# Performance work log

Hardware: AMD Instinct MI355X
Metric: run time of the kernel (lower is better)

The kernel has to match this reference:

```python
import jax, jax.numpy as jnp
import numpy as np

VOCAB = 100000
SHORTLIST = 10000  # cutoffs = [10000, 20000, 40000, 80000], n_clusters = 4
B, T, D = 1024, 128, 1024


def setup_inputs() -> dict:
    key = jax.random.key(0)
    ks = jax.random.split(key, 12)
    s = 0.02  # realistic init scale for weights
    inp = {
        "features": jax.random.normal(ks[0], (B, D), jnp.float32),
        "head_weight": jax.random.normal(ks[1], (SHORTLIST + 4, D), jnp.float32) * s,
        "proj0": jax.random.normal(ks[2], (512, D), jnp.float32) * s,
        "out0": jax.random.normal(ks[3], (10000, 512), jnp.float32) * s,
        "proj1": jax.random.normal(ks[4], (256, D), jnp.float32) * s,
        "out1": jax.random.normal(ks[5], (20000, 256), jnp.float32) * s,
        "proj2": jax.random.normal(ks[6], (128, D), jnp.float32) * s,
        "out2": jax.random.normal(ks[7], (40000, 128), jnp.float32) * s,
        "proj3": jax.random.normal(ks[8], (64, D), jnp.float32) * s,
        "out3": jax.random.normal(ks[9], (20000, 64), jnp.float32) * s,
        "discard_probs": jax.random.uniform(ks[10], (VOCAB,), jnp.float32),
        "targets": jax.random.randint(ks[11], (B, T), 0, VOCAB, jnp.int64),
        "target_mask": jnp.ones((B, T), jnp.bool_),
    }
    return inp


def _adaptive_log_prob(x, head_weight, projs, outs):
    # head: shortlist logits + one logit per tail cluster
    head_lp = jax.nn.log_softmax(x @ head_weight.T, axis=-1)  # [B, SHORTLIST+4]
    parts = [head_lp[:, :SHORTLIST]]
    for i, (pw, ow) in enumerate(zip(projs, outs)):
        cluster_logits = (x @ pw.T) @ ow.T  # [B, osz]
        parts.append(jax.nn.log_softmax(cluster_logits, axis=-1)
                     + head_lp[:, SHORTLIST + i:SHORTLIST + i + 1])
    return jnp.concatenate(parts, axis=-1)  # [B, VOCAB]


def reference(features, head_weight, proj0, out0, proj1, out1, proj2, out2,
              proj3, out3, discard_probs, targets, target_mask):
    # dropout is identity in eval/reference mode
    logprob = _adaptive_log_prob(features, head_weight,
                                 (proj0, proj1, proj2, proj3),
                                 (out0, out1, out2, out3))
    lp_t = jnp.take_along_axis(logprob, targets, axis=1)        # [B, T]
    w = (1.0 - discard_probs[targets]) * target_mask.astype(lp_t.dtype)
    per_sample = jnp.sum(-lp_t * w, axis=1) / jnp.sum(w, axis=1)  # [B]
    return jnp.sum(per_sample) / (targets.shape[0] + 1e-5)
```

## Files before the change

kernel.cpp:

```cpp
#include <hip/hip_runtime.h>
#include <cstdint>


typedef unsigned short u16;
typedef __attribute__((ext_vector_type(4))) float f32x4;
typedef __attribute__((ext_vector_type(8))) __bf16 bf16x8;
typedef __attribute__((ext_vector_type(4))) unsigned int u32x4;

__device__ __forceinline__ u16 f2bf(float f){
  unsigned u = __float_as_uint(f);
  u += 0x7FFFu + ((u >> 16) & 1u);
  return (u16)(u >> 16);
}

__device__ __forceinline__ float wave_sum(float v){
  #pragma unroll
  for (int d = 1; d < 64; d <<= 1) v += __shfl_xor(v, d, 64);
  return v;
}

__device__ __forceinline__ float wave_dot_l(const u16* a_lds, const u16* b, int len, int lane){
  float s = 0.f;
  for (int k = lane*8; k < len; k += 512){
    u32x4 va = *(const u32x4*)(a_lds + k);
    u32x4 vb = *(const u32x4*)(b + k);
    #pragma unroll
    for (int i = 0; i < 4; i++){
      unsigned ua = va[i], ub = vb[i];
      s = fmaf(__uint_as_float(ua << 16),        __uint_as_float(ub << 16),        s);
      s = fmaf(__uint_as_float(ua & 0xFFFF0000u), __uint_as_float(ub & 0xFFFF0000u), s);
    }
  }
  return wave_sum(s);
}

__device__ __forceinline__ void gload_lds16(const void* g, void* l){
  __builtin_amdgcn_global_load_lds(
      (const __attribute__((address_space(1))) unsigned int*)g,
      (__attribute__((address_space(3))) unsigned int*)l, 16, 0, 0);
}

struct CvtSeg { const float* src; u16* dst; unsigned start; };
struct CvtTab { CvtSeg s[10]; unsigned total; };

__global__ __launch_bounds__(256) void cvt_bf16(CvtTab t){
  unsigned stride = gridDim.x * blockDim.x;
  for (unsigned c = blockIdx.x*blockDim.x + threadIdx.x; c < t.total; c += stride){
    int si = 0;
    #pragma unroll
    for (int i = 1; i < 10; i++) if (c >= t.s[i].start) si = i;
    unsigned lo = c - t.s[si].start;
    const float4* sp = (const float4*)t.s[si].src + (size_t)lo*2;
    float4 f0 = sp[0], f1 = sp[1];
    uint4 d;
    d.x = (unsigned)f2bf(f0.x) | ((unsigned)f2bf(f0.y) << 16);
    d.y = (unsigned)f2bf(f0.z) | ((unsigned)f2bf(f0.w) << 16);
    d.z = (unsigned)f2bf(f1.x) | ((unsigned)f2bf(f1.y) << 16);
    d.w = (unsigned)f2bf(f1.z) | ((unsigned)f2bf(f1.w) << 16);
    ((uint4*)t.s[si].dst)[lo] = d;
  }
}

struct GSeg { const u16* A; const u16* B; float* part; u16* C; float* gates;
              int lda, N, K, ntiles, tileStart, ldc; };
struct GTab { GSeg seg[5]; int nseg; int swz; };

__global__ __launch_bounds__(256, 4) void gemm_all(GTab tab){
  __shared__ __attribute__((aligned(16))) u16 ldsA[128*64];
  __shared__ __attribute__((aligned(16))) u16 ldsB[128*64];
  __shared__ float msLds[128][2];

  int bx = blockIdx.x, by = blockIdx.y;
  if (tab.swz){
    int flat = by * 8 + bx;
    int xcd = flat & 7, j = flat >> 3;
    by = (j >> 3) * 8 + xcd;
    bx = j & 7;
    int nby = (int)gridDim.y;
    if (by >= nby){ by = nby - 1; bx = xcd; }
  }

  int s = 0;
  #pragma unroll
  for (int i = 1; i < 5; i++)
    if (i < tab.nseg && by >= tab.seg[i].tileStart) s = i;
  const u16* Ab = tab.seg[s].A;
  const u16* Bb = tab.seg[s].B;
  float* part   = tab.seg[s].part;
  u16* Cc       = tab.seg[s].C;
  float* gatesp = tab.seg[s].gates;
  int lda = tab.seg[s].lda, N = tab.seg[s].N, K = tab.seg[s].K;
  int ntiles = tab.seg[s].ntiles, ldc = tab.seg[s].ldc;
  int tileN = by - tab.seg[s].tileStart;
  int n0 = tileN * 128;
  int row0 = bx * 128;

  int tid = threadIdx.x;
  int wid = tid >> 6, lane = tid & 63;
  int wr = wid >> 1, wc = wid & 1;
  int qr = lane >> 4, ln = lane & 15;

  const char* baseA = (const char*)(Ab + (size_t)row0*lda);
  const char* baseB = (const char*)Bb;
  unsigned offA[4], offB[4];
  #pragma unroll
  for (int t = 0; t < 4; t++){
    int c = t*256 + tid, row = c >> 3, jj = (c & 7) ^ (row & 7);
    offA[t] = (unsigned)(row*lda + jj*8) * 2u;
    int nr = n0 + row; if (nr >= N) nr = N - 1;
    offB[t] = (unsigned)(nr*K + jj*8) * 2u;
  }
  unsigned ldsWave = (unsigned)(wid << 6) * 16u;

  f32x4 acc[4][4];
  const f32x4 zero = {0.f, 0.f, 0.f, 0.f};
  #pragma unroll
  for (int i = 0; i < 4; i++)
    #pragma unroll
    for (int j = 0; j < 4; j++) acc[i][j] = zero;

  int nkt = K >> 6;
  for (int kt = 0; kt < nkt; kt++){
    __syncthreads();
    unsigned kb = (unsigned)kt * 128u;
    #pragma unroll
    for (int t = 0; t < 4; t++){
      gload_lds16(baseA + offA[t] + kb, (char*)ldsA + (unsigned)t*4096u + ldsWave);
      gload_lds16(baseB + offB[t] + kb, (char*)ldsB + (unsigned)t*4096u + ldsWave);
    }
    __syncthreads();
    #pragma unroll
    for (int ks = 0; ks < 2; ks++){
      bf16x8 av[4], bv[4];
      #pragma unroll
      for (int mt = 0; mt < 4; mt++){
        int rl = wr*64 + mt*16 + ln;
        int ch = rl*8 + ((ks*4 + qr) ^ (rl & 7));
        av[mt] = *(const bf16x8*)((const char*)ldsA + ch*16);
      }
      #pragma unroll
      for (int nt = 0; nt < 4; nt++){
        int rl = wc*64 + nt*16 + ln;
        int ch = rl*8 + ((ks*4 + qr) ^ (rl & 7));
        bv[nt] = *(const bf16x8*)((const char*)ldsB + ch*16);
      }
      #pragma unroll
      for (int mt = 0; mt < 4; mt++)
        #pragma unroll
        for (int nt = 0; nt < 4; nt++)
          acc[mt][nt] = __builtin_amdgcn_mfma_f32_16x16x32_bf16(av[mt], bv[nt], acc[mt][nt], 0, 0, 0);
    }
  }

  if (part){
    #pragma unroll
    for (int mt = 0; mt < 4; mt++){
      #pragma unroll
      for (int r = 0; r < 4; r++){
        float ss = 0.f;
        #pragma unroll
        for (int nt = 0; nt < 4; nt++){
          int col = n0 + wc*64 + nt*16 + ln;
          if (col < N){
            float v = acc[mt][nt][r];
            ss += __expf(v);
            if (gatesp && col >= 10000){
              int row = row0 + wr*64 + mt*16 + qr*4 + r;
              gatesp[row*4 + (col - 10000)] = v;
            }
          }
        }
        ss += __shfl_xor(ss, 1, 64);
        ss += __shfl_xor(ss, 2, 64);
        ss += __shfl_xor(ss, 4, 64);
        ss += __shfl_xor(ss, 8, 64);
        if (ln == 0) msLds[wr*64 + mt*16 + qr*4 + r][wc] = ss;
      }
    }
    __syncthreads();
    if (tid < 128)
      part[(size_t)(row0 + tid)*ntiles + tileN] = msLds[tid][0] + msLds[tid][1];
  } else {
    #pragma unroll
    for (int mt = 0; mt < 4; mt++)
      #pragma unroll
      for (int nt = 0; nt < 4; nt++)
        #pragma unroll
        for (int r = 0; r < 4; r++){
          int col = n0 + wc*64 + nt*16 + ln;
          if (col < N){
            int row = row0 + wr*64 + mt*16 + qr*4 + r;
            Cc[(size_t)row*ldc + col] = f2bf(acc[mt][nt][r]);
          }
        }
  }
}

struct LseTab { const float* base[5]; int ntiles[5]; float* lse; };

__global__ __launch_bounds__(256) void lse_reduce(LseTab t){
  int widx = blockIdx.x*4 + (threadIdx.x >> 6);
  int lane = threadIdx.x & 63;
  int mat = widx >> 10, row = widx & 1023;
  const float* p = t.base[mat] + (size_t)row * t.ntiles[mat];
  float s = 0.f;
  for (int i = lane; i < t.ntiles[mat]; i += 64) s += p[i];
  s = wave_sum(s);
  if (lane == 0) t.lse[mat*1024 + row] = __logf(s);
}

struct GatherArgs {
  const u16* Xb; const u16* Hb; const u16* Hact; const u16* Ob;
  const float* lse; const float* gates; const int* targets;
  const float* discard; float* psamp;
};

__global__ __launch_bounds__(256) void gather_rows(GatherArgs g){
  __shared__ __attribute__((aligned(16))) u16 xr[1024];
  __shared__ __attribute__((aligned(16))) u16 hr[960];
  __shared__ __attribute__((aligned(16))) int tg[128];
  __shared__ float ls[5], gs[4];
  __shared__ float lpv[128];
  __shared__ float sa[2], sw[2];

  int b = blockIdx.x;
  int tid = threadIdx.x;
  int w = tid >> 6, lane = tid & 63;

  if (tid < 128) ((u32x4*)xr)[tid] = ((const u32x4*)(g.Xb + (size_t)b*1024))[tid];
  else if (tid < 248) ((u32x4*)hr)[tid-128] = ((const u32x4*)(g.Hact + (size_t)b*960))[tid-128];
  if (tid < 32) ((u32x4*)tg)[tid] = ((const u32x4*)(g.targets + (size_t)b*128))[tid];
  if (tid < 5) ls[tid] = g.lse[tid*1024 + b];
  if (tid < 4) gs[tid] = g.gates[b*4 + tid];
  __syncthreads();

  for (int t = 0; t < 32; t++){
    int ti = w*32 + t;
    int v = tg[ti];
    float val;
    if (v < 10000){
      float logit = wave_dot_l(xr, g.Hb + (size_t)v*1024, 1024, lane);
      val = logit - ls[0];
    } else {
      int c, off, psz, hoff; size_t oboff;
      if      (v < 20000){ c=0; off=10000; psz=512; hoff=0;   oboff=0; }
      else if (v < 40000){ c=1; off=20000; psz=256; hoff=512; oboff=5120000; }
      else if (v < 80000){ c=2; off=40000; psz=128; hoff=768; oboff=10240000; }
      else               { c=3; off=80000; psz=64;  hoff=896; oboff=15360000; }
      float logit = wave_dot_l(hr + hoff, g.Ob + oboff + (size_t)(v - off)*psz, psz, lane);
      val = gs[c] - ls[0] + logit - ls[c + 1];
    }
    if (lane == 0) lpv[ti] = val;
  }
  __syncthreads();

  if (tid < 128){
    int v = tg[tid];
    float wt = 1.0f - g.discard[v];
    float a  = -lpv[tid] * wt;
    float as = wave_sum(a), ws = wave_sum(wt);
    if (lane == 0){ sa[w] = as; sw[w] = ws; }
  }
  __syncthreads();
  if (tid == 0) g.psamp[b] = (sa[0] + sa[1]) / (sw[0] + sw[1]);
}

__global__ __launch_bounds__(256) void final_sum(const float* psamp, float* out){
  float s = 0.f;
  for (int i = threadIdx.x; i < 1024; i += 256) s += psamp[i];
  s = wave_sum(s);
  __shared__ float sb[4];
  if ((threadIdx.x & 63) == 0) sb[threadIdx.x >> 6] = s;
  __syncthreads();
  if (threadIdx.x == 0) out[0] = (sb[0] + sb[1] + sb[2] + sb[3]) / (1024.0f + 1e-5f);
}

extern "C" void kernel_launch(void* const* d_in, const int* in_sizes, int n_in,
                              void* d_out, int out_size, void* d_ws, size_t ws_size,
                              hipStream_t stream){
  (void)in_sizes; (void)n_in; (void)out_size; (void)ws_size;
  const float* features = (const float*)d_in[0];
  const float* head_w   = (const float*)d_in[1];
  const float* proj[4]  = {(const float*)d_in[2], (const float*)d_in[4],
                           (const float*)d_in[6], (const float*)d_in[8]};
  const float* outw[4]  = {(const float*)d_in[3], (const float*)d_in[5],
                           (const float*)d_in[7], (const float*)d_in[9]};
  const float* discard  = (const float*)d_in[10];
  const int*   targets  = (const int*)d_in[11];
  float* out = (float*)d_out;

  char* wsp = (char*)d_ws;
  size_t off = 0;
  auto carve = [&](size_t bytes)->char*{
    char* p = wsp + off; off += (bytes + 255) & ~(size_t)255; return p;
  };
  u16* Xb     = (u16*)carve(1024ull*1024*2);
  u16* Hb     = (u16*)carve(10004ull*1024*2);
  u16* Pb     = (u16*)carve(960ull*1024*2);
  u16* Ob     = (u16*)carve(16640000ull*2);
  u16* Hact   = (u16*)carve(1024ull*960*2);
  float* part = (float*)carve(803840ull*4);
  float* lse  = (float*)carve(5*1024*4);
  float* gates= (float*)carve(4096*4);
  float* psamp= (float*)carve(1024*4);

  CvtTab ct{};
  const float* srcs[10] = {features, head_w, proj[0], proj[1], proj[2], proj[3],
                           outw[0], outw[1], outw[2], outw[3]};
  u16* dsts[10] = {Xb, Hb, Pb, Pb + 512*1024, Pb + 768*1024, Pb + 896*1024,
                   Ob, Ob + 5120000, Ob + 10240000, Ob + 15360000};
  unsigned counts[10] = {1048576u, 10244096u, 524288u, 262144u, 131072u, 65536u,
                         5120000u, 5120000u, 5120000u, 1280000u};
  unsigned pre = 0;
  for (int i = 0; i < 10; i++){
    ct.s[i].src = srcs[i]; ct.s[i].dst = dsts[i]; ct.s[i].start = pre;
    pre += counts[i] / 8;
  }
  ct.total = pre;
  cvt_bf16<<<dim3(4096), dim3(256), 0, stream>>>(ct);

  float* pHead = part;
  float* pC0 = part + 80896;
  float* pC1 = part + 161792;
  float* pC2 = part + 322560;
  float* pC3 = part + 643072;

  GTab tp{};
  tp.nseg = 4; tp.swz = 0;
  tp.seg[0] = {Xb, Pb,            nullptr, Hact,       nullptr, 1024, 512, 1024, 4, 0, 960};
  tp.seg[1] = {Xb, Pb + 512*1024, nullptr, Hact + 512, nullptr, 1024, 256, 1024, 2, 4, 960};
  tp.seg[2] = {Xb, Pb + 768*1024, nullptr, Hact + 768, nullptr, 1024, 128, 1024, 1, 6, 960};
  tp.seg[3] = {Xb, Pb + 896*1024, nullptr, Hact + 896, nullptr, 1024, 64,  1024, 1, 7, 960};
  gemm_all<<<dim3(8, 8), dim3(256), 0, stream>>>(tp);

  GTab tm{};
  tm.nseg = 5; tm.swz = 1;
  tm.seg[0] = {Xb,         Hb,            pHead, nullptr, gates,   1024, 10004, 1024, 79,  0,   0};
  tm.seg[1] = {Hact,       Ob,            pC0,   nullptr, nullptr, 960,  10000, 512,  79,  79,  0};
  tm.seg[2] = {Hact + 512, Ob + 5120000,  pC1,   nullptr, nullptr, 960,  20000, 256,  157, 158, 0};
  tm.seg[3] = {Hact + 768, Ob + 10240000, pC2,   nullptr, nullptr, 960,  40000, 128,  313, 315, 0};
  tm.seg[4] = {Hact + 896, Ob + 15360000, pC3,   nullptr, nullptr, 960,  20000, 64,   157, 628, 0};
  gemm_all<<<dim3(8, 785), dim3(256), 0, stream>>>(tm);

  LseTab lt{};
  lt.base[0] = pHead; lt.base[1] = pC0; lt.base[2] = pC1; lt.base[3] = pC2; lt.base[4] = pC3;
  lt.ntiles[0] = 79; lt.ntiles[1] = 79; lt.ntiles[2] = 157; lt.ntiles[3] = 313; lt.ntiles[4] = 157;
  lt.lse = lse;
  lse_reduce<<<dim3(1280), dim3(256), 0, stream>>>(lt);

  GatherArgs ga{Xb, Hb, Hact, Ob, lse, gates, targets, discard, psamp};
  gather_rows<<<dim3(1024), dim3(256), 0, stream>>>(ga);

  final_sum<<<dim3(1), dim3(256), 0, stream>>>(psamp, out);
}
```

Before: 297.0 us.

## Add persistent A-stationary GEMM for small-K tail clusters and transpose partial sums

Splits the clusters with small inner dimension (K=128 and K=64) out of the main GEMM launch into a new kernel. That kernel keeps the full A tile resident in LDS and loops over several consecutive N tiles per block, restaging only B each time. The aim is to cut repeated A loads, per-tile launch and sync overhead, and the short K loops that are poorly amortised. Partial sum-of-exp buffers are stored tile-major so writes and the lse_reduce reads coalesce, and lse_reduce now uses one thread per row. The trade-offs are fewer blocks in the persistent grid (lower parallelism), no overlap between staging B and the MFMA work, and serial per-thread reduction loops.

```diff
diff --git a/kernel.cpp b/kernel.cpp
--- a/kernel.cpp
+++ b/kernel.cpp
@@ -76,8 +76,7 @@
     int xcd = flat & 7, j = flat >> 3;
     by = (j >> 3) * 8 + xcd;
     bx = j & 7;
-    int nby = (int)gridDim.y;
-    if (by >= nby){ by = nby - 1; bx = xcd; }
+    if (by >= (int)gridDim.y){ by = j; bx = xcd; }
   }
 
   int s = 0;
@@ -90,7 +89,7 @@
   u16* Cc       = tab.seg[s].C;
   float* gatesp = tab.seg[s].gates;
   int lda = tab.seg[s].lda, N = tab.seg[s].N, K = tab.seg[s].K;
-  int ntiles = tab.seg[s].ntiles, ldc = tab.seg[s].ldc;
+  int ldc = tab.seg[s].ldc;
   int tileN = by - tab.seg[s].tileStart;
   int n0 = tileN * 128;
   int row0 = bx * 128;
@@ -110,7 +109,6 @@
     int nr = n0 + row; if (nr >= N) nr = N - 1;
     offB[t] = (unsigned)(nr*K + jj*8) * 2u;
   }
-  unsigned ldsWave = (unsigned)(wid << 6) * 16u;
 
   f32x4 acc[4][4];
   const f32x4 zero = {0.f, 0.f, 0.f, 0.f};
@@ -125,8 +123,8 @@
     unsigned kb = (unsigned)kt * 128u;
     #pragma unroll
     for (int t = 0; t < 4; t++){
-      gload_lds16(baseA + offA[t] + kb, (char*)ldsA + (unsigned)t*4096u + ldsWave);
-      gload_lds16(baseB + offB[t] + kb, (char*)ldsB + (unsigned)t*4096u + ldsWave);
+      gload_lds16(baseA + offA[t] + kb, (char*)ldsA + (size_t)(t*256 + tid)*16);
+      gload_lds16(baseB + offB[t] + kb, (char*)ldsB + (size_t)(t*256 + tid)*16);
     }
     __syncthreads();
     #pragma unroll
@@ -179,7 +177,7 @@
     }
     __syncthreads();
     if (tid < 128)
-      part[(size_t)(row0 + tid)*ntiles + tileN] = msLds[tid][0] + msLds[tid][1];
+      part[(size_t)tileN*1024 + row0 + tid] = msLds[tid][0] + msLds[tid][1];
   } else {
     #pragma unroll
     for (int mt = 0; mt < 4; mt++)
@@ -196,17 +194,129 @@
   }
 }
 
+struct PSeg { const u16* A; const u16* B; float* part; int N, K, ntiles, byStart, cpb; };
+struct PTab { PSeg seg[2]; int nby; };
+
+__global__ __launch_bounds__(256, 2) void gemm_apersist(PTab tab){
+  __shared__ __attribute__((aligned(16))) u16 ldsA[128*128];
+  __shared__ __attribute__((aligned(16))) u16 ldsB[128*128];
+  __shared__ float msLds[128][2];
+
+  int bx = blockIdx.x, by = blockIdx.y;
+  {
+    int flat = by * 8 + bx;
+    int xcd = flat & 7, j = flat >> 3;
+    by = (j >> 3) * 8 + xcd;
+    bx = j & 7;
+    if (by >= tab.nby){ by = j; bx = xcd; }
+  }
+  int s = (by >= tab.seg[1].byStart) ? 1 : 0;
+  const u16* Ab = tab.seg[s].A;
+  const u16* Bb = tab.seg[s].B;
+  float* part   = tab.seg[s].part;
+  int N = tab.seg[s].N, K = tab.seg[s].K;
+  int ntiles = tab.seg[s].ntiles, cpb = tab.seg[s].cpb;
+  int nkt = K >> 6;
+  int ct0 = (by - tab.seg[s].byStart) * cpb;
+  int ctCnt = ntiles - ct0; if (ctCnt > cpb) ctCnt = cpb;
+  int row0 = bx * 128;
+  const int lda = 960;
+
+  int tid = threadIdx.x;
+  int wid = tid >> 6, lane = tid & 63;
+  int wr = wid >> 1, wc = wid & 1;
+  int qr = lane >> 4, ln = lane & 15;
+
+  for (int i = 0; i < nkt*4; i++){
+    int c = i*256 + tid;
+    int cl = c & 1023, kt = c >> 10;
+    int row = cl >> 3, jj = (cl & 7) ^ (row & 7);
+    gload_lds16(Ab + (size_t)(row0 + row)*lda + kt*64 + jj*8,
+                (char*)ldsA + (size_t)c*16);
+  }
+  auto stageB = [&](int tg){
+    int n0 = tg * 128;
+    for (int i = 0; i < nkt*4; i++){
+      int c = i*256 + tid;
+      int cl = c & 1023, kt = c >> 10;
+      int row = cl >> 3, jj = (cl & 7) ^ (row & 7);
+      int nr = n0 + row; if (nr >= N) nr = N - 1;
+      gload_lds16(Bb + (size_t)nr*K + kt*64 + jj*8,
+                  (char*)ldsB + (size_t)c*16);
+    }
+  };
+  stageB(ct0);
+  __syncthreads();
+
+  for (int ct = 0; ct < ctCnt; ct++){
+    int tg = ct0 + ct, n0 = tg * 128;
+
+    f32x4 acc[4][4];
+    const f32x4 zero = {0.f, 0.f, 0.f, 0.f};
+    #pragma unroll
+    for (int i = 0; i < 4; i++)
+      #pragma unroll
+      for (int j = 0; j < 4; j++) acc[i][j] = zero;
+
+    for (int kt = 0; kt < nkt; kt++){
+      #pragma unroll
+      for (int ks = 0; ks < 2; ks++){
+        bf16x8 av[4], bv[4];
+        #pragma unroll
+        for (int mt = 0; mt < 4; mt++){
+          int rl = wr*64 + mt*16 + ln;
+          int ch = rl*8 + ((ks*4 + qr) ^ (rl & 7));
+          av[mt] = *(const bf16x8*)((const char*)ldsA + (size_t)kt*16384 + ch*16);
+        }
+        #pragma unroll
+        for (int nt = 0; nt < 4; nt++){
+          int rl = wc*64 + nt*16 + ln;
+          int ch = rl*8 + ((ks*4 + qr) ^ (rl & 7));
+          bv[nt] = *(const bf16x8*)((const char*)ldsB + (size_t)kt*16384 + ch*16);
+        }
+        #pragma unroll
+        for (int mt = 0; mt < 4; mt++)
+          #pragma unroll
+          for (int nt = 0; nt < 4; nt++)
+            acc[mt][nt] = __builtin_amdgcn_mfma_f32_16x16x32_bf16(av[mt], bv[nt], acc[mt][nt], 0, 0, 0);
+      }
+    }
+
+    #pragma unroll
+    for (int mt = 0; mt < 4; mt++){
+      #pragma unroll
+      for (int r = 0; r < 4; r++){
+        float ss = 0.f;
+        #pragma unroll
+        for (int nt = 0; nt < 4; nt++){
+          int col = n0 + wc*64 + nt*16 + ln;
+          if (col < N) ss += __expf(acc[mt][nt][r]);
+        }
+        ss += __shfl_xor(ss, 1, 64);
+        ss += __shfl_xor(ss, 2, 64);
+        ss += __shfl_xor(ss, 4, 64);
+        ss += __shfl_xor(ss, 8, 64);
+        if (ln == 0) msLds[wr*64 + mt*16 + qr*4 + r][wc] = ss;
+      }
+    }
+    __syncthreads();
+    if (tid < 128)
+      part[(size_t)tg*1024 + row0 + tid] = msLds[tid][0] + msLds[tid][1];
+    if (ct + 1 < ctCnt) stageB(tg + 1);
+    __syncthreads();
+  }
+}
+
 struct LseTab { const float* base[5]; int ntiles[5]; float* lse; };
 
 __global__ __launch_bounds__(256) void lse_reduce(LseTab t){
-  int widx = blockIdx.x*4 + (threadIdx.x >> 6);
-  int lane = threadIdx.x & 63;
-  int mat = widx >> 10, row = widx & 1023;
-  const float* p = t.base[mat] + (size_t)row * t.ntiles[mat];
+  int g = blockIdx.x*256 + threadIdx.x;
+  int mat = g >> 10, row = g & 1023;
+  const float* p = t.base[mat] + row;
+  int n = t.ntiles[mat];
   float s = 0.f;
-  for (int i = lane; i < t.ntiles[mat]; i += 64) s += p[i];
-  s = wave_sum(s);
-  if (lane == 0) t.lse[mat*1024 + row] = __logf(s);
+  for (int i = 0; i < n; i++) s += p[(size_t)i*1024];
+  t.lse[g] = __logf(s);
 }
 
 struct GatherArgs {
@@ -334,19 +444,23 @@
   gemm_all<<<dim3(8, 8), dim3(256), 0, stream>>>(tp);
 
   GTab tm{};
-  tm.nseg = 5; tm.swz = 1;
-  tm.seg[0] = {Xb,         Hb,            pHead, nullptr, gates,   1024, 10004, 1024, 79,  0,   0};
-  tm.seg[1] = {Hact,       Ob,            pC0,   nullptr, nullptr, 960,  10000, 512,  79,  79,  0};
-  tm.seg[2] = {Hact + 512, Ob + 5120000,  pC1,   nullptr, nullptr, 960,  20000, 256,  157, 158, 0};
-  tm.seg[3] = {Hact + 768, Ob + 10240000, pC2,   nullptr, nullptr, 960,  40000, 128,  313, 315, 0};
-  tm.seg[4] = {Hact + 896, Ob + 15360000, pC3,   nullptr, nullptr, 960,  20000, 64,   157, 628, 0};
-  gemm_all<<<dim3(8, 785), dim3(256), 0, stream>>>(tm);
+  tm.nseg = 3; tm.swz = 1;
+  tm.seg[0] = {Xb,         Hb,           pHead, nullptr, gates,   1024, 10004, 1024, 79,  0,   0};
+  tm.seg[1] = {Hact,       Ob,           pC0,   nullptr, nullptr, 960,  10000, 512,  79,  79,  0};
+  tm.seg[2] = {Hact + 512, Ob + 5120000, pC1,   nullptr, nullptr, 960,  20000, 256,  157, 158, 0};
+  gemm_all<<<dim3(8, 315), dim3(256), 0, stream>>>(tm);
+
+  PTab pm{};
+  pm.nby = 60;
+  pm.seg[0] = {Hact + 768, Ob + 10240000, pC2, 40000, 128, 313, 0,  8};
+  pm.seg[1] = {Hact + 896, Ob + 15360000, pC3, 20000, 64,  157, 40, 8};
+  gemm_apersist<<<dim3(8, 60), dim3(256), 0, stream>>>(pm);
 
   LseTab lt{};
   lt.base[0] = pHead; lt.base[1] = pC0; lt.base[2] = pC1; lt.base[3] = pC2; lt.base[4] = pC3;
   lt.ntiles[0] = 79; lt.ntiles[1] = 79; lt.ntiles[2] = 157; lt.ntiles[3] = 313; lt.ntiles[4] = 157;
   lt.lse = lse;
-  lse_reduce<<<dim3(1280), dim3(256), 0, stream>>>(lt);
+  lse_reduce<<<dim3(20), dim3(256), 0, stream>>>(lt);
 
   GatherArgs ga{Xb, Hb, Hact, Ob, lse, gates, targets, discard, psamp};
   gather_rows<<<dim3(1024), dim3(256), 0, stream>>>(ga);
```

Result: slower. 386.7 us (+30.2%).

## Fuse projection GEMM into conversion kernel and fold LSE reduction into gather

Applied to the files above, without the earlier changes.

The projection GEMM now runs inside the bf16 conversion kernel: the first 64 blocks read fp32 features and projection weights directly, convert them in registers and compute Hact, while the remaining blocks convert the other weights. The separate lse_reduce kernel is removed. The main GEMM writes partial exp-sums in tile-major layout, and gather_rows sums them and takes the log itself. This cuts two kernel launches and the intermediate projection-weight buffer. In exchange, projection tiles use synchronous fp32 loads instead of async LDS loads, and every gather block does a strided reduction over 785 partial values.

```diff
diff --git a/kernel.cpp b/kernel.cpp
--- a/kernel.cpp
+++ b/kernel.cpp
@@ -11,6 +11,15 @@
   unsigned u = __float_as_uint(f);
   u += 0x7FFFu + ((u >> 16) & 1u);
   return (u16)(u >> 16);
+}
+
+__device__ __forceinline__ uint4 pack_bf16x8(float4 f0, float4 f1){
+  uint4 d;
+  d.x = (unsigned)f2bf(f0.x) | ((unsigned)f2bf(f0.y) << 16);
+  d.y = (unsigned)f2bf(f0.z) | ((unsigned)f2bf(f0.w) << 16);
+  d.z = (unsigned)f2bf(f1.x) | ((unsigned)f2bf(f1.y) << 16);
+  d.w = (unsigned)f2bf(f1.z) | ((unsigned)f2bf(f1.w) << 16);
+  return d;
 }
 
 __device__ __forceinline__ float wave_sum(float v){
@@ -41,29 +50,113 @@
 }
 
 struct CvtSeg { const float* src; u16* dst; unsigned start; };
-struct CvtTab { CvtSeg s[10]; unsigned total; };
-
-__global__ __launch_bounds__(256) void cvt_bf16(CvtTab t){
-  unsigned stride = gridDim.x * blockDim.x;
-  for (unsigned c = blockIdx.x*blockDim.x + threadIdx.x; c < t.total; c += stride){
-    int si = 0;
-    #pragma unroll
-    for (int i = 1; i < 10; i++) if (c >= t.s[i].start) si = i;
-    unsigned lo = c - t.s[si].start;
-    const float4* sp = (const float4*)t.s[si].src + (size_t)lo*2;
-    float4 f0 = sp[0], f1 = sp[1];
-    uint4 d;
-    d.x = (unsigned)f2bf(f0.x) | ((unsigned)f2bf(f0.y) << 16);
-    d.y = (unsigned)f2bf(f0.z) | ((unsigned)f2bf(f0.w) << 16);
-    d.z = (unsigned)f2bf(f1.x) | ((unsigned)f2bf(f1.y) << 16);
-    d.w = (unsigned)f2bf(f1.z) | ((unsigned)f2bf(f1.w) << 16);
-    ((uint4*)t.s[si].dst)[lo] = d;
-  }
-}
-
-struct GSeg { const u16* A; const u16* B; float* part; u16* C; float* gates;
-              int lda, N, K, ntiles, tileStart, ldc; };
-struct GTab { GSeg seg[5]; int nseg; int swz; };
+struct PjSeg  { const float* B; u16* C; int N, tileStart; };
+struct CPArgs {
+  CvtSeg cs[6]; unsigned total;
+  const float* Af32;
+  PjSeg pseg[4];
+};
+
+__global__ __launch_bounds__(256) void cvt_proj(CPArgs a){
+  __shared__ __attribute__((aligned(16))) u16 ldsA[128*64];
+  __shared__ __attribute__((aligned(16))) u16 ldsB[128*64];
+
+  int tid = threadIdx.x;
+
+  if (blockIdx.x >= 64){
+    unsigned stride = (gridDim.x - 64) * 256u;
+    for (unsigned c = (blockIdx.x - 64)*256u + tid; c < a.total; c += stride){
+      int si = 0;
+      #pragma unroll
+      for (int i = 1; i < 6; i++) if (c >= a.cs[i].start) si = i;
+      unsigned lo = c - a.cs[si].start;
+      const float4* sp = (const float4*)a.cs[si].src + (size_t)lo*2;
+      ((uint4*)a.cs[si].dst)[lo] = pack_bf16x8(sp[0], sp[1]);
+    }
+    return;
+  }
+
+  int bxr = blockIdx.x & 7, byc = blockIdx.x >> 3;
+  int s = 0;
+  #pragma unroll
+  for (int i = 1; i < 4; i++) if (byc >= a.pseg[i].tileStart) s = i;
+  const float* Bf = a.pseg[s].B;
+  u16* Cc = a.pseg[s].C;
+  int N = a.pseg[s].N;
+  int n0 = (byc - a.pseg[s].tileStart) * 128;
+  int row0 = bxr * 128;
+
+  int wid = tid >> 6, lane = tid & 63;
+  int wr = wid >> 1, wc = wid & 1;
+  int qr = lane >> 4, ln = lane & 15;
+
+  int rrow[4], jjj[4]; unsigned nrB[4];
+  #pragma unroll
+  for (int t = 0; t < 4; t++){
+    int c = t*256 + tid, row = c >> 3, jj = (c & 7) ^ (row & 7);
+    rrow[t] = row; jjj[t] = jj;
+    int nr = n0 + row; if (nr >= N) nr = N - 1;
+    nrB[t] = (unsigned)nr;
+  }
+
+  f32x4 acc[4][4];
+  const f32x4 zero = {0.f, 0.f, 0.f, 0.f};
+  #pragma unroll
+  for (int i = 0; i < 4; i++)
+    #pragma unroll
+    for (int j = 0; j < 4; j++) acc[i][j] = zero;
+
+  for (int kt = 0; kt < 16; kt++){
+    __syncthreads();
+    #pragma unroll
+    for (int t = 0; t < 4; t++){
+      int c = t*256 + tid;
+      const float4* sa = (const float4*)(a.Af32 + (size_t)(row0 + rrow[t])*1024 + kt*64 + jjj[t]*8);
+      *(uint4*)((char*)ldsA + (size_t)c*16) = pack_bf16x8(sa[0], sa[1]);
+      const float4* sb = (const float4*)(Bf + (size_t)nrB[t]*1024 + kt*64 + jjj[t]*8);
+      *(uint4*)((char*)ldsB + (size_t)c*16) = pack_bf16x8(sb[0], sb[1]);
+    }
+    __syncthreads();
+    #pragma unroll
+    for (int ks = 0; ks < 2; ks++){
+      bf16x8 av[4], bv[4];
+      #pragma unroll
+      for (int mt = 0; mt < 4; mt++){
+        int rl = wr*64 + mt*16 + ln;
+        int ch = rl*8 + ((ks*4 + qr) ^ (rl & 7));
+        av[mt] = *(const bf16x8*)((const char*)ldsA + ch*16);
+      }
+      #pragma unroll
+      for (int nt = 0; nt < 4; nt++){
+        int rl = wc*64 + nt*16 + ln;
+        int ch = rl*8 + ((ks*4 + qr) ^ (rl & 7));
+        bv[nt] = *(const bf16x8*)((const char*)ldsB + ch*16);
+      }
+      #pragma unroll
+      for (int mt = 0; mt < 4; mt++)
+        #pragma unroll
+        for (int nt = 0; nt < 4; nt++)
+          acc[mt][nt] = __builtin_amdgcn_mfma_f32_16x16x32_bf16(av[mt], bv[nt], acc[mt][nt], 0, 0, 0);
+    }
+  }
+
+  #pragma unroll
+  for (int mt = 0; mt < 4; mt++)
+    #pragma unroll
+    for (int nt = 0; nt < 4; nt++)
+      #pragma unroll
+      for (int r = 0; r < 4; r++){
+        int col = n0 + wc*64 + nt*16 + ln;
+        if (col < N){
+          int row = row0 + wr*64 + mt*16 + qr*4 + r;
+          Cc[(size_t)row*960 + col] = f2bf(acc[mt][nt][r]);
+        }
+      }
+}
+
+struct GSeg { const u16* A; const u16* B; float* part; float* gates;
+              int lda, N, K, tileStart; };
+struct GTab { GSeg seg[5]; };
 
 __global__ __launch_bounds__(256, 4) void gemm_all(GTab tab){
   __shared__ __attribute__((aligned(16))) u16 ldsA[128*64];
@@ -71,26 +164,23 @@
   __shared__ float msLds[128][2];
 
   int bx = blockIdx.x, by = blockIdx.y;
-  if (tab.swz){
+  {
     int flat = by * 8 + bx;
     int xcd = flat & 7, j = flat >> 3;
     by = (j >> 3) * 8 + xcd;
     bx = j & 7;
-    int nby = (int)gridDim.y;
-    if (by >= nby){ by = nby - 1; bx = xcd; }
+    if (by >= (int)gridDim.y){ by = j; bx = xcd; }
   }
 
   int s = 0;
   #pragma unroll
   for (int i = 1; i < 5; i++)
-    if (i < tab.nseg && by >= tab.seg[i].tileStart) s = i;
+    if (by >= tab.seg[i].tileStart) s = i;
   const u16* Ab = tab.seg[s].A;
   const u16* Bb = tab.seg[s].B;
   float* part   = tab.seg[s].part;
-  u16* Cc       = tab.seg[s].C;
   float* gatesp = tab.seg[s].gates;
   int lda = tab.seg[s].lda, N = tab.seg[s].N, K = tab.seg[s].K;
-  int ntiles = tab.seg[s].ntiles, ldc = tab.seg[s].ldc;
   int tileN = by - tab.seg[s].tileStart;
   int n0 = tileN * 128;
   int row0 = bx * 128;
@@ -110,7 +200,6 @@
     int nr = n0 + row; if (nr >= N) nr = N - 1;
     offB[t] = (unsigned)(nr*K + jj*8) * 2u;
   }
-  unsigned ldsWave = (unsigned)(wid << 6) * 16u;
 
   f32x4 acc[4][4];
   const f32x4 zero = {0.f, 0.f, 0.f, 0.f};
@@ -125,8 +214,8 @@
     unsigned kb = (unsigned)kt * 128u;
     #pragma unroll
     for (int t = 0; t < 4; t++){
-      gload_lds16(baseA + offA[t] + kb, (char*)ldsA + (unsigned)t*4096u + ldsWave);
-      gload_lds16(baseB + offB[t] + kb, (char*)ldsB + (unsigned)t*4096u + ldsWave);
+      gload_lds16(baseA + offA[t] + kb, (char*)ldsA + (size_t)(t*256 + tid)*16);
+      gload_lds16(baseB + offB[t] + kb, (char*)ldsB + (size_t)(t*256 + tid)*16);
     }
     __syncthreads();
     #pragma unroll
@@ -152,66 +241,38 @@
     }
   }
 
-  if (part){
-    #pragma unroll
-    for (int mt = 0; mt < 4; mt++){
-      #pragma unroll
-      for (int r = 0; r < 4; r++){
-        float ss = 0.f;
-        #pragma unroll
-        for (int nt = 0; nt < 4; nt++){
-          int col = n0 + wc*64 + nt*16 + ln;
-          if (col < N){
-            float v = acc[mt][nt][r];
-            ss += __expf(v);
-            if (gatesp && col >= 10000){
-              int row = row0 + wr*64 + mt*16 + qr*4 + r;
-              gatesp[row*4 + (col - 10000)] = v;
-            }
+  #pragma unroll
+  for (int mt = 0; mt < 4; mt++){
+    #pragma unroll
+    for (int r = 0; r < 4; r++){
+      float ss = 0.f;
+      #pragma unroll
+      for (int nt = 0; nt < 4; nt++){
+        int col = n0 + wc*64 + nt*16 + ln;
+        if (col < N){
+          float v = acc[mt][nt][r];
+          ss += __expf(v);
+          if (gatesp && col >= 10000){
+            int row = row0 + wr*64 + mt*16 + qr*4 + r;
+            gatesp[row*4 + (col - 10000)] = v;
           }
         }
-        ss += __shfl_xor(ss, 1, 64);
-        ss += __shfl_xor(ss, 2, 64);
-        ss += __shfl_xor(ss, 4, 64);
-        ss += __shfl_xor(ss, 8, 64);
-        if (ln == 0) msLds[wr*64 + mt*16 + qr*4 + r][wc] = ss;
-      }
-    }
-    __syncthreads();
-    if (tid < 128)
-      part[(size_t)(row0 + tid)*ntiles + tileN] = msLds[tid][0] + msLds[tid][1];
-  } else {
-    #pragma unroll
-    for (int mt = 0; mt < 4; mt++)
-      #pragma unroll
-      for (int nt = 0; nt < 4; nt++)
-        #pragma unroll
-        for (int r = 0; r < 4; r++){
-          int col = n0 + wc*64 + nt*16 + ln;
-          if (col < N){
-            int row = row0 + wr*64 + mt*16 + qr*4 + r;
-            Cc[(size_t)row*ldc + col] = f2bf(acc[mt][nt][r]);
-          }
-        }
-  }
-}
-
-struct LseTab { const float* base[5]; int ntiles[5]; float* lse; };
-
-__global__ __launch_bounds__(256) void lse_reduce(LseTab t){
-  int widx = blockIdx.x*4 + (threadIdx.x >> 6);
-  int lane = threadIdx.x & 63;
-  int mat = widx >> 10, row = widx & 1023;
-  const float* p = t.base[mat] + (size_t)row * t.ntiles[mat];
-  float s = 0.f;
-  for (int i = lane; i < t.ntiles[mat]; i += 64) s += p[i];
-  s = wave_sum(s);
-  if (lane == 0) t.lse[mat*1024 + row] = __logf(s);
+      }
+      ss += __shfl_xor(ss, 1, 64);
+      ss += __shfl_xor(ss, 2, 64);
+      ss += __shfl_xor(ss, 4, 64);
+      ss += __shfl_xor(ss, 8, 64);
+      if (ln == 0) msLds[wr*64 + mt*16 + qr*4 + r][wc] = ss;
+    }
+  }
+  __syncthreads();
+  if (tid < 128)
+    part[(size_t)tileN*1024 + row0 + tid] = msLds[tid][0] + msLds[tid][1];
 }
 
 struct GatherArgs {
   const u16* Xb; const u16* Hb; const u16* Hact; const u16* Ob;
-  const float* lse; const float* gates; const int* targets;
+  const float* part; const float* gates; const int* targets;
   const float* discard; float* psamp;
 };
 
@@ -219,6 +280,7 @@
   __shared__ __attribute__((aligned(16))) u16 xr[1024];
   __shared__ __attribute__((aligned(16))) u16 hr[960];
   __shared__ __attribute__((aligned(16))) int tg[128];
+  __shared__ float sLse[4][5];
   __shared__ float ls[5], gs[4];
   __shared__ float lpv[128];
   __shared__ float sa[2], sw[2];
@@ -230,8 +292,25 @@
   if (tid < 128) ((u32x4*)xr)[tid] = ((const u32x4*)(g.Xb + (size_t)b*1024))[tid];
   else if (tid < 248) ((u32x4*)hr)[tid-128] = ((const u32x4*)(g.Hact + (size_t)b*960))[tid-128];
   if (tid < 32) ((u32x4*)tg)[tid] = ((const u32x4*)(g.targets + (size_t)b*128))[tid];
-  if (tid < 5) ls[tid] = g.lse[tid*1024 + b];
   if (tid < 4) gs[tid] = g.gates[b*4 + tid];
+
+  float p0=0.f, p1=0.f, p2=0.f, p3=0.f, p4=0.f;
+  for (int j = tid; j < 785; j += 256){
+    float v = g.part[(size_t)j*1024 + b];
+    if      (j <  79) p0 += v;
+    else if (j < 158) p1 += v;
+    else if (j < 315) p2 += v;
+    else if (j < 628) p3 += v;
+    else              p4 += v;
+  }
+  p0 = wave_sum(p0); p1 = wave_sum(p1); p2 = wave_sum(p2);
+  p3 = wave_sum(p3); p4 = wave_sum(p4);
+  if (lane == 0){
+    sLse[w][0]=p0; sLse[w][1]=p1; sLse[w][2]=p2; sLse[w][3]=p3; sLse[w][4]=p4;
+  }
+  __syncthreads();
+  if (tid < 5)
+    ls[tid] = __logf(sLse[0][tid] + sLse[1][tid] + sLse[2][tid] + sLse[3][tid]);
   __syncthreads();
 
   for (int t = 0; t < 32; t++){
@@ -296,28 +375,30 @@
   };
   u16* Xb     = (u16*)carve(1024ull*1024*2);
   u16* Hb     = (u16*)carve(10004ull*1024*2);
-  u16* Pb     = (u16*)carve(960ull*1024*2);
   u16* Ob     = (u16*)carve(16640000ull*2);
   u16* Hact   = (u16*)carve(1024ull*960*2);
   float* part = (float*)carve(803840ull*4);
-  float* lse  = (float*)carve(5*1024*4);
   float* gates= (float*)carve(4096*4);
   float* psamp= (float*)carve(1024*4);
 
-  CvtTab ct{};
-  const float* srcs[10] = {features, head_w, proj[0], proj[1], proj[2], proj[3],
-                           outw[0], outw[1], outw[2], outw[3]};
-  u16* dsts[10] = {Xb, Hb, Pb, Pb + 512*1024, Pb + 768*1024, Pb + 896*1024,
-                   Ob, Ob + 5120000, Ob + 10240000, Ob + 15360000};
-  unsigned counts[10] = {1048576u, 10244096u, 524288u, 262144u, 131072u, 65536u,
-                         5120000u, 5120000u, 5120000u, 1280000u};
-  unsigned pre = 0;
-  for (int i = 0; i < 10; i++){
-    ct.s[i].src = srcs[i]; ct.s[i].dst = dsts[i]; ct.s[i].start = pre;
-    pre += counts[i] / 8;
-  }
-  ct.total = pre;
-  cvt_bf16<<<dim3(4096), dim3(256), 0, stream>>>(ct);
+  CPArgs cp{};
+  {
+    const float* srcs[6] = {features, head_w, outw[0], outw[1], outw[2], outw[3]};
+    u16* dsts[6] = {Xb, Hb, Ob, Ob + 5120000, Ob + 10240000, Ob + 15360000};
+    unsigned counts[6] = {1048576u, 10244096u, 5120000u, 5120000u, 5120000u, 1280000u};
+    unsigned pre = 0;
+    for (int i = 0; i < 6; i++){
+      cp.cs[i].src = srcs[i]; cp.cs[i].dst = dsts[i]; cp.cs[i].start = pre;
+      pre += counts[i] / 8;
+    }
+    cp.total = pre;
+    cp.Af32 = features;
+    cp.pseg[0] = {proj[0], Hact,       512, 0};
+    cp.pseg[1] = {proj[1], Hact + 512, 256, 4};
+    cp.pseg[2] = {proj[2], Hact + 768, 128, 6};
+    cp.pseg[3] = {proj[3], Hact + 896,  64, 7};
+  }
+  cvt_proj<<<dim3(4160), dim3(256), 0, stream>>>(cp);
 
   float* pHead = part;
   float* pC0 = part + 80896;
@@ -325,30 +406,15 @@
   float* pC2 = part + 322560;
   float* pC3 = part + 643072;
 
-  GTab tp{};
-  tp.nseg = 4; tp.swz = 0;
-  tp.seg[0] = {Xb, Pb,            nullptr, Hact,       nullptr, 1024, 512, 1024, 4, 0, 960};
-  tp.seg[1] = {Xb, Pb + 512*1024, nullptr, Hact + 512, nullptr, 1024, 256, 1024, 2, 4, 960};
-  tp.seg[2] = {Xb, Pb + 768*1024, nullptr, Hact + 768, nullptr, 1024, 128, 1024, 1, 6, 960};
-  tp.seg[3] = {Xb, Pb + 896*1024, nullptr, Hact + 896, nullptr, 1024, 64,  1024, 1, 7, 960};
-  gemm_all<<<dim3(8, 8), dim3(256), 0, stream>>>(tp);
-
   GTab tm{};
-  tm.nseg = 5; tm.swz = 1;
-  tm.seg[0] = {Xb,         Hb,            pHead, nullptr, gates,   1024, 10004, 1024, 79,  0,   0};
-  tm.seg[1] = {Hact,       Ob,            pC0,   nullptr, nullptr, 960,  10000, 512,  79,  79,  0};
-  tm.seg[2] = {Hact + 512, Ob + 5120000,  pC1,   nullptr, nullptr, 960,  20000, 256,  157, 158, 0};
-  tm.seg[3] = {Hact + 768, Ob + 10240000, pC2,   nullptr, nullptr, 960,  40000, 128,  313, 315, 0};
-  tm.seg[4] = {Hact + 896, Ob + 15360000, pC3,   nullptr, nullptr, 960,  20000, 64,   157, 628, 0};
+  tm.seg[0] = {Xb,         Hb,            pHead, gates,   1024, 10004, 1024, 0};
+  tm.seg[1] = {Hact,       Ob,            pC0,   nullptr, 960,  10000, 512,  79};
+  tm.seg[2] = {Hact + 512, Ob + 5120000,  pC1,   nullptr, 960,  20000, 256,  158};
+  tm.seg[3] = {Hact + 768, Ob + 10240000, pC2,   nullptr, 960,  40000, 128,  315};
+  tm.seg[4] = {Hact + 896, Ob + 15360000, pC3,   nullptr, 960,  20000, 64,   628};
   gemm_all<<<dim3(8, 785), dim3(256), 0, stream>>>(tm);
 
-  LseTab lt{};
-  lt.base[0] = pHead; lt.base[1] = pC0; lt.base[2] = pC1; lt.base[3] = pC2; lt.base[4] = pC3;
-  lt.ntiles[0] = 79; lt.ntiles[1] = 79; lt.ntiles[2] = 157; lt.ntiles[3] = 313; lt.ntiles[4] = 157;
-  lt.lse = lse;
-  lse_reduce<<<dim3(1280), dim3(256), 0, stream>>>(lt);
-
-  GatherArgs ga{Xb, Hb, Hact, Ob, lse, gates, targets, discard, psamp};
+  GatherArgs ga{Xb, Hb, Hact, Ob, part, gates, targets, discard, psamp};
   gather_rows<<<dim3(1024), dim3(256), 0, stream>>>(ga);
 
   final_sum<<<dim3(1), dim3(256), 0, stream>>>(psamp, out);
```

Result: slower. 322.9 us (+8.7%).
